# Kernel tuning notes

Hardware: AMD Instinct MI355X
Metric: run time of the kernel (lower is better)

## Reference

```python
import jax, jax.numpy as jnp
import numpy as np

B, N, D = 16384, 64, 64

def setup_inputs() -> dict:
    key = jax.random.key(0)
    ks = jax.random.split(key, 8)
    return {
        "self_vectors": jax.random.normal(ks[0], (B, 1, D), dtype=jnp.float32),
        "neighbor_vectors": jax.random.normal(ks[1], (B, 1, N, D), dtype=jnp.float32),
        "neighbor_relations": jax.random.normal(ks[2], (B, 1, N, D), dtype=jnp.float32),
        "user_embeddings": jax.random.normal(ks[3], (B, D), dtype=jnp.float32),
        "W1": jax.random.normal(ks[4], (2 * D, D), dtype=jnp.float32) * (1.0 / np.sqrt(2 * D)),
        "b1": jnp.zeros((D,), dtype=jnp.float32),
        "w2": jax.random.normal(ks[5], (D, 1), dtype=jnp.float32) * (1.0 / np.sqrt(D)),
        "b2": jnp.zeros((1,), dtype=jnp.float32),
    }

def reference(self_vectors, neighbor_vectors, neighbor_relations, user_embeddings, W1, b1, w2, b2):
    b, _, n, d = neighbor_relations.shape
    # user embedding broadcast over neighbors: [b,1,n,d]
    ue = jnp.broadcast_to(user_embeddings[:, None, None, :], (b, 1, n, d))
    head_rel = jnp.concatenate([ue, neighbor_relations], axis=-1)  # [b,1,n,2d]
    hidden = jax.nn.relu(head_rel @ W1 + b1)                        # [b,1,n,d]
    decay = jax.nn.sigmoid(hidden @ w2 + b2)                        # [b,1,n,1]
    decay = jax.nn.softmax(decay, axis=2)                           # softmax over neighbors
    agg = jnp.sum(decay * neighbor_vectors, axis=2)                 # [b,1,d]
    return jnp.concatenate([self_vectors, agg], axis=-1)           # [b,1,2d]
```

## Files before the change

kernel.cpp:

```cpp
#include <hip/hip_runtime.h>
#include <math.h>

#define BATCH 16384
#define NN 64
#define DD 64
#define RS 65

__global__ __launch_bounds__(256, 8)
void aggregator_kernel(const float* __restrict__ self_v,
                       const float* __restrict__ nv,
                       const float* __restrict__ rel,
                       const float* __restrict__ ue,
                       const float* __restrict__ W1,
                       const float* __restrict__ b1,
                       const float* __restrict__ w2,
                       const float* __restrict__ b2,
                       float* __restrict__ out)
{
    const int b = blockIdx.x;
    const int t = threadIdx.x;
    const int lane = t & 63;
    const int w = __builtin_amdgcn_readfirstlane(t >> 6);

    __shared__ float rel_s[NN * RS];
    __shared__ float u1p_s[4][DD];
    __shared__ float pd_s[4][DD];
    __shared__ float agg_s[4][DD];

    const float* __restrict__ relb = rel + (size_t)b * (NN * DD);

    float4 r[4];
    #pragma unroll
    for (int i = 0; i < 4; ++i) r[i] = ((const float4*)relb)[i * 256 + t];

    {
        const float* __restrict__ ueb = ue + (size_t)b * DD + 16 * w;
        float pu = 0.0f;
        #pragma unroll
        for (int kk = 0; kk < 16; ++kk) {
            pu = fmaf(ueb[kk], W1[(16 * w + kk) * DD + lane], pu);
        }
        u1p_s[w][lane] = pu;
    }

    float sv = 0.0f;
    if (w == 0) sv = self_v[(size_t)b * DD + lane];

    #pragma unroll
    for (int i = 0; i < 4; ++i) {
        int idx = i * 256 + t;
        int n = idx >> 4;
        int k = (idx & 15) * 4;
        float* p = &rel_s[n * RS + k];
        p[0] = r[i].x; p[1] = r[i].y; p[2] = r[i].z; p[3] = r[i].w;
    }
    __syncthreads();

    const float* __restrict__ nvb = nv + (size_t)b * (NN * DD) + (size_t)(16 * w) * DD + lane;
    float nvr[16];
    #pragma unroll
    for (int i = 0; i < 16; ++i) nvr[i] = nvb[(size_t)i * DD];

    float acc[16];
    #pragma unroll
    for (int jj = 0; jj < 16; ++jj) {
        int j = 16 * w + jj;
        acc[jj] = b1[j] + u1p_s[0][j] + u1p_s[1][j] + u1p_s[2][j] + u1p_s[3][j];
    }

    const float* __restrict__ Wq = W1 + DD * DD + 16 * w;
    #pragma unroll 4
    for (int k = 0; k < DD; ++k) {
        float x = rel_s[lane * RS + k];
        const float* __restrict__ row = Wq + (size_t)k * DD;
        #pragma unroll
        for (int jj = 0; jj < 16; ++jj) acc[jj] = fmaf(x, row[jj], acc[jj]);
    }

    {
        const float* __restrict__ w2q = w2 + 16 * w;
        float pd = 0.0f;
        #pragma unroll
        for (int jj = 0; jj < 16; ++jj) pd = fmaf(fmaxf(acc[jj], 0.0f), w2q[jj], pd);
        pd_s[w][lane] = pd;
    }
    __syncthreads();

    float d = b2[0] + pd_s[0][lane] + pd_s[1][lane] + pd_s[2][lane] + pd_s[3][lane];
    float dec = 1.0f / (1.0f + __expf(-d));
    float m = dec;
    #pragma unroll
    for (int off = 32; off > 0; off >>= 1) m = fmaxf(m, __shfl_xor(m, off, 64));
    float e = __expf(dec - m);
    float s = e;
    #pragma unroll
    for (int off = 32; off > 0; off >>= 1) s += __shfl_xor(s, off, 64);
    float wv = e / s;

    float pa = 0.0f;
    #pragma unroll
    for (int i = 0; i < 16; ++i) {
        float wi = __shfl(wv, 16 * w + i, 64);
        pa = fmaf(wi, nvr[i], pa);
    }
    agg_s[w][lane] = pa;

    if (w == 0) out[(size_t)b * (2 * DD) + lane] = sv;
    __syncthreads();

    if (w == 0) {
        out[(size_t)b * (2 * DD) + DD + lane] =
            agg_s[0][lane] + agg_s[1][lane] + agg_s[2][lane] + agg_s[3][lane];
    }
}

extern "C" void kernel_launch(void* const* d_in, const int* in_sizes, int n_in,
                              void* d_out, int out_size, void* d_ws, size_t ws_size,
                              hipStream_t stream) {
    const float* self_v = (const float*)d_in[0];
    const float* nv     = (const float*)d_in[1];
    const float* rel    = (const float*)d_in[2];
    const float* ue     = (const float*)d_in[3];
    const float* W1     = (const float*)d_in[4];
    const float* b1     = (const float*)d_in[5];
    const float* w2     = (const float*)d_in[6];
    const float* b2     = (const float*)d_in[7];
    float* out = (float*)d_out;

    aggregator_kernel<<<dim3(BATCH), dim3(256), 0, stream>>>(
        self_v, nv, rel, ue, W1, b1, w2, b2, out);
}
```

Baseline: 533.0 us.

## Hold W1 slice in registers, broadcast via readlane, prefetch neighbor vectors early

Each lane now loads one row of the relation half of W1 into 16 registers, and the inner matmul loop broadcasts weights with v_readlane instead of issuing scalar/global loads per k. The neighbor vector loads move before the first barrier, with a sched_barrier, so their latency overlaps the user-embedding projection. The softmax-weight shuffles become readlanes, bias/partial sums are read as float4, the unroll rises to 8, and the launch-bounds occupancy hint drops to 6 to give more registers. This trades occupancy and register pressure for fewer memory instructions in the hot loop.

```diff
diff --git a/kernel.cpp b/kernel.cpp
--- a/kernel.cpp
+++ b/kernel.cpp
@@ -6,7 +6,7 @@
 #define DD 64
 #define RS 65
 
-__global__ __launch_bounds__(256, 8)
+__global__ __launch_bounds__(256, 6)
 void aggregator_kernel(const float* __restrict__ self_v,
                        const float* __restrict__ nv,
                        const float* __restrict__ rel,
@@ -33,6 +33,25 @@
     #pragma unroll
     for (int i = 0; i < 4; ++i) r[i] = ((const float4*)relb)[i * 256 + t];
 
+    float wreg[16];
+    {
+        const float* __restrict__ wrow = W1 + DD * DD + lane * DD + 16 * w;
+        float4 q0 = *(const float4*)(wrow + 0);
+        float4 q1 = *(const float4*)(wrow + 4);
+        float4 q2 = *(const float4*)(wrow + 8);
+        float4 q3 = *(const float4*)(wrow + 12);
+        wreg[0]=q0.x;  wreg[1]=q0.y;  wreg[2]=q0.z;  wreg[3]=q0.w;
+        wreg[4]=q1.x;  wreg[5]=q1.y;  wreg[6]=q1.z;  wreg[7]=q1.w;
+        wreg[8]=q2.x;  wreg[9]=q2.y;  wreg[10]=q2.z; wreg[11]=q2.w;
+        wreg[12]=q3.x; wreg[13]=q3.y; wreg[14]=q3.z; wreg[15]=q3.w;
+    }
+
+    const float* __restrict__ nvb = nv + (size_t)b * (NN * DD) + (size_t)(16 * w) * DD + lane;
+    float nvr[16];
+    #pragma unroll
+    for (int i = 0; i < 16; ++i) nvr[i] = nvb[(size_t)i * DD];
+    __builtin_amdgcn_sched_barrier(0);
+
     {
         const float* __restrict__ ueb = ue + (size_t)b * DD + 16 * w;
         float pu = 0.0f;
@@ -56,25 +75,27 @@
     }
     __syncthreads();
 
-    const float* __restrict__ nvb = nv + (size_t)b * (NN * DD) + (size_t)(16 * w) * DD + lane;
-    float nvr[16];
-    #pragma unroll
-    for (int i = 0; i < 16; ++i) nvr[i] = nvb[(size_t)i * DD];
-
     float acc[16];
     #pragma unroll
-    for (int jj = 0; jj < 16; ++jj) {
-        int j = 16 * w + jj;
-        acc[jj] = b1[j] + u1p_s[0][j] + u1p_s[1][j] + u1p_s[2][j] + u1p_s[3][j];
+    for (int q = 0; q < 4; ++q) {
+        float4 a = *(const float4*)(b1 + 16 * w + 4 * q);
+        #pragma unroll
+        for (int p = 0; p < 4; ++p) {
+            float4 u = *(const float4*)&u1p_s[p][16 * w + 4 * q];
+            a.x += u.x; a.y += u.y; a.z += u.z; a.w += u.w;
+        }
+        acc[4*q+0] = a.x; acc[4*q+1] = a.y; acc[4*q+2] = a.z; acc[4*q+3] = a.w;
     }
 
-    const float* __restrict__ Wq = W1 + DD * DD + 16 * w;
-    #pragma unroll 4
+    #pragma unroll 8
     for (int k = 0; k < DD; ++k) {
         float x = rel_s[lane * RS + k];
-        const float* __restrict__ row = Wq + (size_t)k * DD;
         #pragma unroll
-        for (int jj = 0; jj < 16; ++jj) acc[jj] = fmaf(x, row[jj], acc[jj]);
+        for (int jj = 0; jj < 16; ++jj) {
+            float wk = __int_as_float(
+                __builtin_amdgcn_readlane(__float_as_int(wreg[jj]), k));
+            acc[jj] = fmaf(x, wk, acc[jj]);
+        }
     }
 
     {
@@ -100,7 +121,8 @@
     float pa = 0.0f;
     #pragma unroll
     for (int i = 0; i < 16; ++i) {
-        float wi = __shfl(wv, 16 * w + i, 64);
+        float wi = __int_as_float(
+            __builtin_amdgcn_readlane(__float_as_int(wv), 16 * w + i));
         pa = fmaf(wi, nvr[i], pa);
     }
     agg_s[w][lane] = pa;
```

After: 763.5 us. +43.3%, slower.
